# Kernel tuning notes

Hardware: AMD Instinct MI355X
Metric: run time of the kernel (lower is better)

Reference implementation:

```python
import jax, jax.numpy as jnp
import numpy as np

N = 100000      # nodes
E = 1600000     # edges (avg degree 16)
D_IN, D_HID, D_OUT = 128, 64, 32


def setup_inputs() -> dict:
    key = jax.random.key(0)
    ks = jax.random.split(key, 11)
    g = lambda k, shape, fan: jax.random.normal(k, shape, jnp.float32) * (1.0 / np.sqrt(fan))
    return {
        "x": jax.random.normal(ks[0], (N, D_IN), jnp.float32),
        "edges_index": jax.random.randint(ks[1], (2, E), 0, N, dtype=jnp.int64),
        # GATConv layer 1 (heads=1): linear weight, attention vectors a_src/a_dst, bias
        "W1": g(ks[2], (D_IN, D_HID), D_IN),
        "a_src1": g(ks[3], (D_HID,), D_HID),
        "a_dst1": g(ks[4], (D_HID,), D_HID),
        "b1": jnp.zeros((D_HID,), jnp.float32),
        # GATConv layer 2
        "W2": g(ks[5], (D_HID, D_OUT), D_HID),
        "a_src2": g(ks[6], (D_OUT,), D_OUT),
        "a_dst2": g(ks[7], (D_OUT,), D_OUT),
        "b2": jnp.zeros((D_OUT,), jnp.float32),
    }


def _gat_conv(x, src, dst, W, a_src, a_dst, b, n):
    """Single-head PyG GATConv: transform, edge attention, per-dst softmax, scatter-add."""
    h = x @ W                                        # [N, D]
    e = jax.nn.leaky_relu((h @ a_src)[src] + (h @ a_dst)[dst], 0.2)  # [E']
    # segment softmax over edges grouped by destination node
    m = jax.ops.segment_max(e, dst, num_segments=n)  # [N]
    w = jnp.exp(e - m[dst])                          # [E']
    s = jax.ops.segment_sum(w, dst, num_segments=n)  # [N]
    att = w / (s[dst] + 1e-16)                       # [E']
    out = jax.ops.segment_sum(att[:, None] * h[src], dst, num_segments=n)  # [N, D]
    return out + b


def reference(x, edges_index, W1, a_src1, a_dst1, b1, W2, a_src2, a_dst2, b2):
    n = x.shape[0]
    loops = jnp.arange(n, dtype=edges_index.dtype)   # GATConv add_self_loops=True
    src = jnp.concatenate([edges_index[0], loops])
    dst = jnp.concatenate([edges_index[1], loops])
    h = jax.nn.relu(_gat_conv(x, src, dst, W1, a_src1, a_dst1, b1, n))
    # F.dropout with training=False is identity (eval mode)
    out = _gat_conv(h, src, dst, W2, a_src2, a_dst2, b2, n)
    return jax.nn.log_softmax(out, axis=1)
```

## Files before the change

kernel.cpp:

```cpp
#include <hip/hip_runtime.h>
#include <math.h>

#define D_IN 128
#define D_HID 64
#define D_OUT 32
#define CAP 48
#define BSH 8
#define NB 391
#define CAPB 4608
#define CHUNK 8192
#define NPW 4

typedef __fp16 half2f __attribute__((ext_vector_type(2)));

__device__ __forceinline__ half2f u2h2(unsigned u) {
    union { unsigned u; half2f h; } c; c.u = u; return c.h;
}
__device__ __forceinline__ unsigned h22u(half2f h) {
    union { half2f h; unsigned u; } c; c.h = h; return c.u;
}
__device__ __forceinline__ unsigned short f2h(float f) {
    union { _Float16 h; unsigned short u; } c; c.h = (_Float16)f; return c.u;
}

#if defined(__has_builtin)
#  if __has_builtin(__builtin_amdgcn_fdot2)
#    define HAVE_FDOT2 1
#  else
#    define HAVE_FDOT2 0
#  endif
#else
#  define HAVE_FDOT2 0
#endif

__device__ __forceinline__ float fdot2f(half2f a, half2f b, float c) {
#if HAVE_FDOT2
    return __builtin_amdgcn_fdot2(a, b, c, false);
#else
    return fmaf((float)a.y, (float)b.y, fmaf((float)a.x, (float)b.x, c));
#endif
}

__device__ __forceinline__ void pair_acc(float wA, float wB, uint2 hA, uint2 hB,
                                         float& a0, float& a1, float& a2, float& a3)
{
    half2f wp = __builtin_amdgcn_cvt_pkrtz(wA, wB);
    a0 = fdot2f(wp, u2h2(__builtin_amdgcn_perm(hB.x, hA.x, 0x05040100u)), a0);
    a1 = fdot2f(wp, u2h2(__builtin_amdgcn_perm(hB.x, hA.x, 0x07060302u)), a1);
    a2 = fdot2f(wp, u2h2(__builtin_amdgcn_perm(hB.y, hA.y, 0x05040100u)), a2);
    a3 = fdot2f(wp, u2h2(__builtin_amdgcn_perm(hB.y, hA.y, 0x07060302u)), a3);
}


__global__ __launch_bounds__(256) void init_kernel(
    int* __restrict__ cnt, int* __restrict__ cursor, int n)
{
    int i = blockIdx.x * 256 + threadIdx.x;
    if (i < n) cnt[i] = 0;
    if (i < NB) cursor[i] = i * CAPB;
}

__global__ __launch_bounds__(256) void part_kernel(
    const int* __restrict__ esrc, const int* __restrict__ edst,
    unsigned long long* __restrict__ ebuf, int* __restrict__ cursor,
    int E, int Et)
{
    __shared__ int hist[NB];
    __shared__ int ofs[NB];
    const int t = threadIdx.x;
    const int base = blockIdx.x * CHUNK;
    const int end = min(base + CHUNK, Et);

    for (int b = t; b < NB; b += 256) hist[b] = 0;
    __syncthreads();
    for (int i = base + t; i < end; i += 256) {
        int d = (i < E) ? edst[i] : (i - E);
        atomicAdd(&hist[d >> BSH], 1);
    }
    __syncthreads();
    for (int b = t; b < NB; b += 256) {
        int c = hist[b];
        ofs[b] = c ? atomicAdd(&cursor[b], c) : 0;
    }
    __syncthreads();
    for (int i = base + t; i < end; i += 256) {
        int d = (i < E) ? edst[i] : (i - E);
        int s = (i < E) ? esrc[i] : (i - E);
        int p = atomicAdd(&ofs[d >> BSH], 1);
        ebuf[p] = ((unsigned long long)(unsigned)s << 32) | (unsigned)d;
    }
}

__global__ __launch_bounds__(256) void fill_bucket_kernel(
    const unsigned long long* __restrict__ ebuf, const int* __restrict__ cursor,
    int* __restrict__ cnt, int* __restrict__ csr_pad)
{
    int b = blockIdx.x;
    int beg = b * CAPB;
    int end = cursor[b];
    for (int i = beg + threadIdx.x; i < end; i += 256) {
        unsigned long long v = ebuf[i];
        int d = (int)(v & 0xffffffffu);
        int s = (int)(v >> 32);
        int slot = atomicAdd(&cnt[d], 1);
        if (slot < CAP) csr_pad[(size_t)d * CAP + slot] = s;
    }
}


template<int K, int NC, int RT, int PAD>
__global__ __launch_bounds__(256) void gemm_alpha_kernel(
    const float* __restrict__ A, const float* __restrict__ W,
    const float* __restrict__ a_src, const float* __restrict__ a_dst,
    unsigned short* __restrict__ C, float* __restrict__ as_,
    float* __restrict__ ad_, int M)
{
    constexpr int TM = 64;
    constexpr int CT = 4;
    constexpr int CG = NC / CT;
    constexpr int KS = K + PAD;
    __shared__ float xs[TM * KS];
    __shared__ float ws[K * NC];
    const int t = threadIdx.x;

    for (int i = t; i < K * NC / 4; i += 256)
        ((float4*)ws)[i] = ((const float4*)W)[i];

    const int base = blockIdx.x * TM;
    for (int i = t; i < TM * K / 4; i += 256) {
        int nloc = i / (K / 4);
        int k4   = i % (K / 4);
        int row  = base + nloc;
        float4 v = make_float4(0.f, 0.f, 0.f, 0.f);
        if (row < M)
            v = *(const float4*)(A + (size_t)row * K + k4 * 4);
        *(float4*)(xs + nloc * KS + k4 * 4) = v;
    }
    __syncthreads();

    const int tx = t % CG, ty = t / CG;
    const int r0 = ty * RT, c0 = tx * CT;
    float acc[RT][CT];
#pragma unroll
    for (int i = 0; i < RT; ++i)
#pragma unroll
        for (int j = 0; j < CT; ++j) acc[i][j] = 0.f;

    for (int k = 0; k < K; k += 4) {
        float4 a[RT];
#pragma unroll
        for (int i = 0; i < RT; ++i)
            a[i] = *(const float4*)(xs + (r0 + i) * KS + k);
#pragma unroll
        for (int kk = 0; kk < 4; ++kk) {
            float4 b = *(const float4*)(ws + (k + kk) * NC + c0);
#pragma unroll
            for (int i = 0; i < RT; ++i) {
                float av = kk == 0 ? a[i].x : kk == 1 ? a[i].y :
                           kk == 2 ? a[i].z : a[i].w;
                acc[i][0] = fmaf(av, b.x, acc[i][0]);
                acc[i][1] = fmaf(av, b.y, acc[i][1]);
                acc[i][2] = fmaf(av, b.z, acc[i][2]);
                acc[i][3] = fmaf(av, b.w, acc[i][3]);
            }
        }
    }

    const float4 asv = *(const float4*)(a_src + c0);
    const float4 adv = *(const float4*)(a_dst + c0);
#pragma unroll
    for (int i = 0; i < RT; ++i) {
        int row = base + r0 + i;
        float ps = acc[i][0] * asv.x + acc[i][1] * asv.y +
                   acc[i][2] * asv.z + acc[i][3] * asv.w;
        float pd = acc[i][0] * adv.x + acc[i][1] * adv.y +
                   acc[i][2] * adv.z + acc[i][3] * adv.w;
#pragma unroll
        for (int o = 1; o < CG; o <<= 1) {
            ps += __shfl_xor(ps, o);
            pd += __shfl_xor(pd, o);
        }
        if (row < M) {
            uint2 cv;
            cv.x = h22u(__builtin_amdgcn_cvt_pkrtz(acc[i][0], acc[i][1]));
            cv.y = h22u(__builtin_amdgcn_cvt_pkrtz(acc[i][2], acc[i][3]));
            *(uint2*)(C + (size_t)row * NC + c0) = cv;
            if (tx == 0) { as_[row] = ps; ad_[row] = pd; }
        }
    }
}

__global__ __launch_bounds__(256) void gat_aggr_fused_kernel(
    const int* __restrict__ cnt, const int* __restrict__ csr_pad,
    const float* __restrict__ as1, const float* __restrict__ ad1,
    const unsigned short* __restrict__ h1, const float* __restrict__ b1,
    const float* __restrict__ W2, const float* __restrict__ a2s,
    const float* __restrict__ a2d, unsigned short* __restrict__ h2,
    float* __restrict__ as2, float* __restrict__ ad2, int n)
{
    __shared__ float rbuf[4][64];
    const int t = threadIdx.x;
    const int wave = t >> 6;
    const int lane = t & 63;
    const int half = lane >> 5, j = lane & 31;

    float w2r[32];
#pragma unroll
    for (int k = 0; k < 32; ++k)
        w2r[k] = W2[(size_t)(half * 32 + k) * D_OUT + j];
    const float a2sj = a2s[j], a2dj = a2d[j];

    const int sub = lane >> 4;
    const int q4 = (lane & 15) * 4;
    const unsigned short* hq = h1 + q4;
    const float4 b1v = *(const float4*)(b1 + q4);

    const int d0 = (blockIdx.x * 4 + wave) * NPW;
    for (int it = 0; it < NPW; ++it) {
        const int d = d0 + it;
        if (d >= n) break;
        const int deg = min(cnt[d], CAP);
        const float add = ad1[d];

        int s = 0; float e = -1e30f;
        if (lane < deg) {
            s = csr_pad[(size_t)d * CAP + lane];
            float ev = as1[s] + add;
            e = (ev > 0.f) ? ev : 0.2f * ev;
        }
        float m = e;
#pragma unroll
        for (int o = 32; o > 0; o >>= 1) m = fmaxf(m, __shfl_xor(m, o));
        float w = __expf(e - m);
        float ssum = w;

        float a0 = 0.f, a1 = 0.f, a2v = 0.f, a3 = 0.f;
        {
            const int i0 = sub;
            float wA = __shfl(w, i0),      wB = __shfl(w, i0 + 4);
            float wC = __shfl(w, i0 + 8),  wD = __shfl(w, i0 + 12);
            int   sA = __shfl(s, i0),      sB = __shfl(s, i0 + 4);
            int   sC = __shfl(s, i0 + 8),  sD = __shfl(s, i0 + 12);
            uint2 hA = *(const uint2*)(hq + (size_t)sA * 64);
            uint2 hB = *(const uint2*)(hq + (size_t)sB * 64);
            uint2 hC = *(const uint2*)(hq + (size_t)sC * 64);
            uint2 hD = *(const uint2*)(hq + (size_t)sD * 64);
            if (deg > 16) {
                float wE = __shfl(w, i0 + 16), wF = __shfl(w, i0 + 20);
                float wG = __shfl(w, i0 + 24), wH = __shfl(w, i0 + 28);
                int   sE = __shfl(s, i0 + 16), sF = __shfl(s, i0 + 20);
                int   sG = __shfl(s, i0 + 24), sH = __shfl(s, i0 + 28);
                uint2 hE = *(const uint2*)(hq + (size_t)sE * 64);
                uint2 hF = *(const uint2*)(hq + (size_t)sF * 64);
                uint2 hG = *(const uint2*)(hq + (size_t)sG * 64);
                uint2 hH = *(const uint2*)(hq + (size_t)sH * 64);
                pair_acc(wA, wB, hA, hB, a0, a1, a2v, a3);
                pair_acc(wC, wD, hC, hD, a0, a1, a2v, a3);
                pair_acc(wE, wF, hE, hF, a0, a1, a2v, a3);
                pair_acc(wG, wH, hG, hH, a0, a1, a2v, a3);
            } else {
                pair_acc(wA, wB, hA, hB, a0, a1, a2v, a3);
                pair_acc(wC, wD, hC, hD, a0, a1, a2v, a3);
            }
        }
        if (deg > 32) {
            for (int tt = 32; tt < deg; tt += 16) {
                const int i0 = tt + sub;
                float wA = __shfl(w, i0),     wB = __shfl(w, i0 + 4);
                float wC = __shfl(w, i0 + 8), wD = __shfl(w, i0 + 12);
                int   sA = __shfl(s, i0),     sB = __shfl(s, i0 + 4);
                int   sC = __shfl(s, i0 + 8), sD = __shfl(s, i0 + 12);
                uint2 hA = *(const uint2*)(hq + (size_t)sA * 64);
                uint2 hB = *(const uint2*)(hq + (size_t)sB * 64);
                uint2 hC = *(const uint2*)(hq + (size_t)sC * 64);
                uint2 hD = *(const uint2*)(hq + (size_t)sD * 64);
                pair_acc(wA, wB, hA, hB, a0, a1, a2v, a3);
                pair_acc(wC, wD, hC, hD, a0, a1, a2v, a3);
            }
        }

#pragma unroll
        for (int o = 16; o <= 32; o <<= 1) {
            a0 += __shfl_xor(a0, o);  a1 += __shfl_xor(a1, o);
            a2v += __shfl_xor(a2v, o); a3 += __shfl_xor(a3, o);
        }
#pragma unroll
        for (int o = 32; o > 0; o >>= 1) ssum += __shfl_xor(ssum, o);

        const float inv = 1.0f / (ssum + 1e-16f);
        float4 rv;
        rv.x = fmaxf(fmaf(a0, inv, b1v.x), 0.f);
        rv.y = fmaxf(fmaf(a1, inv, b1v.y), 0.f);
        rv.z = fmaxf(fmaf(a2v, inv, b1v.z), 0.f);
        rv.w = fmaxf(fmaf(a3, inv, b1v.w), 0.f);
        if (sub == 0) *(float4*)(&rbuf[wave][q4]) = rv;

        const float* rb = &rbuf[wave][half * 32];
        float acc2 = 0.f;
#pragma unroll
        for (int k4 = 0; k4 < 8; ++k4) {
            float4 r4 = *(const float4*)(rb + k4 * 4);
            acc2 = fmaf(r4.x, w2r[k4 * 4 + 0], acc2);
            acc2 = fmaf(r4.y, w2r[k4 * 4 + 1], acc2);
            acc2 = fmaf(r4.z, w2r[k4 * 4 + 2], acc2);
            acc2 = fmaf(r4.w, w2r[k4 * 4 + 3], acc2);
        }
        acc2 += __shfl_xor(acc2, 32);

        float p1 = acc2 * a2sj, p2 = acc2 * a2dj;
#pragma unroll
        for (int o = 16; o > 0; o >>= 1) {
            p1 += __shfl_xor(p1, o);
            p2 += __shfl_xor(p2, o);
        }
        if (lane < 32) h2[(size_t)d * 32 + j] = f2h(acc2);
        if (lane == 0) { as2[d] = p1; ad2[d] = p2; }
    }
}

__global__ __launch_bounds__(256) void gat_aggr32_lsm_kernel(
    const int* __restrict__ cnt, const int* __restrict__ csr_pad,
    const float* __restrict__ as_, const float* __restrict__ ad_,
    const unsigned short* __restrict__ h, const float* __restrict__ bias,
    float* __restrict__ out, int n)
{
    int wave = threadIdx.x >> 6;
    int lane = threadIdx.x & 63;
    int d = blockIdx.x * 4 + wave;
    if (d >= n) return;
    int deg = min(cnt[d], CAP);
    float add = ad_[d];

    int s = 0; float e = -1e30f;
    if (lane < deg) {
        s = csr_pad[(size_t)d * CAP + lane];
        float ev = as_[s] + add;
        e = (ev > 0.f) ? ev : 0.2f * ev;
    }
    float m = e;
#pragma unroll
    for (int o = 32; o > 0; o >>= 1) m = fmaxf(m, __shfl_xor(m, o));
    float w = __expf(e - m);
    float ssum = w;

    const int sub = lane >> 3;
    const int q4 = (lane & 7) * 4;
    const unsigned short* hq = h + q4;
    float a0 = 0.f, a1 = 0.f, a2v = 0.f, a3 = 0.f;
    {
        const int i0 = sub;
        float wA = __shfl(w, i0),      wB = __shfl(w, i0 + 8);
        int   sA = __shfl(s, i0),      sB = __shfl(s, i0 + 8);
        uint2 hA = *(const uint2*)(hq + (size_t)sA * 32);
        uint2 hB = *(const uint2*)(hq + (size_t)sB * 32);
        if (deg > 16) {
            float wC = __shfl(w, i0 + 16), wD = __shfl(w, i0 + 24);
            int   sC = __shfl(s, i0 + 16), sD = __shfl(s, i0 + 24);
            uint2 hC = *(const uint2*)(hq + (size_t)sC * 32);
            uint2 hD = *(const uint2*)(hq + (size_t)sD * 32);
            pair_acc(wA, wB, hA, hB, a0, a1, a2v, a3);
            pair_acc(wC, wD, hC, hD, a0, a1, a2v, a3);
        } else {
            pair_acc(wA, wB, hA, hB, a0, a1, a2v, a3);
        }
    }
    if (deg > 32) {
        for (int tt = 32; tt < deg; tt += 16) {
            const int i0 = tt + sub;
            float wA = __shfl(w, i0), wB = __shfl(w, i0 + 8);
            int   sA = __shfl(s, i0), sB = __shfl(s, i0 + 8);
            uint2 hA = *(const uint2*)(hq + (size_t)sA * 32);
            uint2 hB = *(const uint2*)(hq + (size_t)sB * 32);
            pair_acc(wA, wB, hA, hB, a0, a1, a2v, a3);
        }
    }
#pragma unroll
    for (int o = 8; o <= 32; o <<= 1) {
        a0 += __shfl_xor(a0, o);  a1 += __shfl_xor(a1, o);
        a2v += __shfl_xor(a2v, o); a3 += __shfl_xor(a3, o);
    }
#pragma unroll
    for (int o = 32; o > 0; o >>= 1) ssum += __shfl_xor(ssum, o);

    float inv = 1.0f / (ssum + 1e-16f);
    const float4 bv = *(const float4*)(bias + q4);
    float r0 = fmaf(a0, inv, bv.x), r1 = fmaf(a1, inv, bv.y);
    float r2 = fmaf(a2v, inv, bv.z), r3 = fmaf(a3, inv, bv.w);

    float mx = fmaxf(fmaxf(r0, r1), fmaxf(r2, r3));
#pragma unroll
    for (int o = 1; o <= 4; o <<= 1) mx = fmaxf(mx, __shfl_xor(mx, o));
    float sm = __expf(r0 - mx) + __expf(r1 - mx) +
               __expf(r2 - mx) + __expf(r3 - mx);
#pragma unroll
    for (int o = 1; o <= 4; o <<= 1) sm += __shfl_xor(sm, o);
    float lg = mx + __logf(sm);
    if (sub == 0) {
        float4 ov = make_float4(r0 - lg, r1 - lg, r2 - lg, r3 - lg);
        *(float4*)(out + (size_t)d * 32 + q4) = ov;
    }
}

extern "C" void kernel_launch(void* const* d_in, const int* in_sizes, int n_in,
                              void* d_out, int out_size, void* d_ws, size_t ws_size,
                              hipStream_t stream) {
    const float* x    = (const float*)d_in[0];
    const int*   ei   = (const int*)  d_in[1];
    const float* W1   = (const float*)d_in[2];
    const float* av1s = (const float*)d_in[3];
    const float* av1d = (const float*)d_in[4];
    const float* b1   = (const float*)d_in[5];
    const float* W2   = (const float*)d_in[6];
    const float* av2s = (const float*)d_in[7];
    const float* av2d = (const float*)d_in[8];
    const float* b2   = (const float*)d_in[9];
    float* out = (float*)d_out;

    const int N  = in_sizes[0] / D_IN;
    const int E  = in_sizes[1] / 2;
    const int Et = E + N;
    const int* esrc = ei;
    const int* edst = ei + E;

    float* ws = (float*)d_ws;
    size_t off = 0;
    unsigned short* h1f = (unsigned short*)(ws + off); off += (size_t)N * 32;
    unsigned short* h2f_ = (unsigned short*)(ws + off); off += (size_t)N * 16;
    float* as1_ = ws + off;               off += N;
    float* ad1_ = ws + off;               off += N;
    float* as2_ = ws + off;               off += N;
    float* ad2_ = ws + off;               off += N;
    int* cnt    = (int*)(ws + off);       off += N;
    int* cursor = (int*)(ws + off);       off += NB + 1;
    int* csr_pad = (int*)(ws + off);      off += (size_t)N * CAP;
    if (off & 1) off++;
    unsigned long long* ebuf = (unsigned long long*)(ws + off);
    off += (size_t)NB * CAPB * 2;

    const int tiles  = (N + 63) / 64;
    const int nblk   = (N + 255) / 256;
    const int aggblk = (N + 3) / 4;
    const int fblk   = (N + 4 * NPW - 1) / (4 * NPW);
    const int pblk   = (Et + CHUNK - 1) / CHUNK;

    init_kernel<<<nblk, 256, 0, stream>>>(cnt, cursor, N);
    part_kernel<<<pblk, 256, 0, stream>>>(esrc, edst, ebuf, cursor, E, Et);
    fill_bucket_kernel<<<NB, 256, 0, stream>>>(ebuf, cursor, cnt, csr_pad);

    gemm_alpha_kernel<128, 64, 4, 0><<<tiles, 256, 0, stream>>>(
        x, W1, av1s, av1d, h1f, as1_, ad1_, N);

    gat_aggr_fused_kernel<<<fblk, 256, 0, stream>>>(
        cnt, csr_pad, as1_, ad1_, h1f, b1,
        W2, av2s, av2d, h2f_, as2_, ad2_, N);

    gat_aggr32_lsm_kernel<<<aggblk, 256, 0, stream>>>(
        cnt, csr_pad, as2_, ad2_, h2f_, b2, out, N);
}
```

Baseline: 311.6 us.

## Process two destination nodes per wave to overlap gather latency

```diff
diff --git a/kernel.cpp b/kernel.cpp
--- a/kernel.cpp
+++ b/kernel.cpp
@@ -9,7 +9,6 @@
 #define NB 391
 #define CAPB 4608
 #define CHUNK 8192
-#define NPW 4
 
 typedef __fp16 half2f __attribute__((ext_vector_type(2)));
 
@@ -198,7 +197,7 @@
     const float* __restrict__ a2d, unsigned short* __restrict__ h2,
     float* __restrict__ as2, float* __restrict__ ad2, int n)
 {
-    __shared__ float rbuf[4][64];
+    __shared__ float rbuf[4][2][64];
     const int t = threadIdx.x;
     const int wave = t >> 6;
     const int lane = t & 63;
@@ -215,106 +214,173 @@
     const unsigned short* hq = h1 + q4;
     const float4 b1v = *(const float4*)(b1 + q4);
 
-    const int d0 = (blockIdx.x * 4 + wave) * NPW;
-    for (int it = 0; it < NPW; ++it) {
-        const int d = d0 + it;
-        if (d >= n) break;
-        const int deg = min(cnt[d], CAP);
-        const float add = ad1[d];
-
-        int s = 0; float e = -1e30f;
-        if (lane < deg) {
-            s = csr_pad[(size_t)d * CAP + lane];
-            float ev = as1[s] + add;
-            e = (ev > 0.f) ? ev : 0.2f * ev;
-        }
-        float m = e;
-#pragma unroll
-        for (int o = 32; o > 0; o >>= 1) m = fmaxf(m, __shfl_xor(m, o));
-        float w = __expf(e - m);
-        float ssum = w;
-
-        float a0 = 0.f, a1 = 0.f, a2v = 0.f, a3 = 0.f;
-        {
-            const int i0 = sub;
-            float wA = __shfl(w, i0),      wB = __shfl(w, i0 + 4);
-            float wC = __shfl(w, i0 + 8),  wD = __shfl(w, i0 + 12);
-            int   sA = __shfl(s, i0),      sB = __shfl(s, i0 + 4);
-            int   sC = __shfl(s, i0 + 8),  sD = __shfl(s, i0 + 12);
-            uint2 hA = *(const uint2*)(hq + (size_t)sA * 64);
-            uint2 hB = *(const uint2*)(hq + (size_t)sB * 64);
-            uint2 hC = *(const uint2*)(hq + (size_t)sC * 64);
-            uint2 hD = *(const uint2*)(hq + (size_t)sD * 64);
-            if (deg > 16) {
-                float wE = __shfl(w, i0 + 16), wF = __shfl(w, i0 + 20);
-                float wG = __shfl(w, i0 + 24), wH = __shfl(w, i0 + 28);
-                int   sE = __shfl(s, i0 + 16), sF = __shfl(s, i0 + 20);
-                int   sG = __shfl(s, i0 + 24), sH = __shfl(s, i0 + 28);
-                uint2 hE = *(const uint2*)(hq + (size_t)sE * 64);
-                uint2 hF = *(const uint2*)(hq + (size_t)sF * 64);
-                uint2 hG = *(const uint2*)(hq + (size_t)sG * 64);
-                uint2 hH = *(const uint2*)(hq + (size_t)sH * 64);
-                pair_acc(wA, wB, hA, hB, a0, a1, a2v, a3);
-                pair_acc(wC, wD, hC, hD, a0, a1, a2v, a3);
-                pair_acc(wE, wF, hE, hF, a0, a1, a2v, a3);
-                pair_acc(wG, wH, hG, hH, a0, a1, a2v, a3);
-            } else {
-                pair_acc(wA, wB, hA, hB, a0, a1, a2v, a3);
-                pair_acc(wC, wD, hC, hD, a0, a1, a2v, a3);
-            }
-        }
-        if (deg > 32) {
-            for (int tt = 32; tt < deg; tt += 16) {
-                const int i0 = tt + sub;
-                float wA = __shfl(w, i0),     wB = __shfl(w, i0 + 4);
-                float wC = __shfl(w, i0 + 8), wD = __shfl(w, i0 + 12);
-                int   sA = __shfl(s, i0),     sB = __shfl(s, i0 + 4);
-                int   sC = __shfl(s, i0 + 8), sD = __shfl(s, i0 + 12);
-                uint2 hA = *(const uint2*)(hq + (size_t)sA * 64);
-                uint2 hB = *(const uint2*)(hq + (size_t)sB * 64);
-                uint2 hC = *(const uint2*)(hq + (size_t)sC * 64);
-                uint2 hD = *(const uint2*)(hq + (size_t)sD * 64);
-                pair_acc(wA, wB, hA, hB, a0, a1, a2v, a3);
-                pair_acc(wC, wD, hC, hD, a0, a1, a2v, a3);
-            }
-        }
-
-#pragma unroll
-        for (int o = 16; o <= 32; o <<= 1) {
-            a0 += __shfl_xor(a0, o);  a1 += __shfl_xor(a1, o);
-            a2v += __shfl_xor(a2v, o); a3 += __shfl_xor(a3, o);
-        }
-#pragma unroll
-        for (int o = 32; o > 0; o >>= 1) ssum += __shfl_xor(ssum, o);
-
-        const float inv = 1.0f / (ssum + 1e-16f);
-        float4 rv;
-        rv.x = fmaxf(fmaf(a0, inv, b1v.x), 0.f);
-        rv.y = fmaxf(fmaf(a1, inv, b1v.y), 0.f);
-        rv.z = fmaxf(fmaf(a2v, inv, b1v.z), 0.f);
-        rv.w = fmaxf(fmaf(a3, inv, b1v.w), 0.f);
-        if (sub == 0) *(float4*)(&rbuf[wave][q4]) = rv;
-
-        const float* rb = &rbuf[wave][half * 32];
-        float acc2 = 0.f;
-#pragma unroll
-        for (int k4 = 0; k4 < 8; ++k4) {
-            float4 r4 = *(const float4*)(rb + k4 * 4);
-            acc2 = fmaf(r4.x, w2r[k4 * 4 + 0], acc2);
-            acc2 = fmaf(r4.y, w2r[k4 * 4 + 1], acc2);
-            acc2 = fmaf(r4.z, w2r[k4 * 4 + 2], acc2);
-            acc2 = fmaf(r4.w, w2r[k4 * 4 + 3], acc2);
-        }
-        acc2 += __shfl_xor(acc2, 32);
-
-        float p1 = acc2 * a2sj, p2 = acc2 * a2dj;
-#pragma unroll
-        for (int o = 16; o > 0; o >>= 1) {
-            p1 += __shfl_xor(p1, o);
-            p2 += __shfl_xor(p2, o);
-        }
-        if (lane < 32) h2[(size_t)d * 32 + j] = f2h(acc2);
-        if (lane == 0) { as2[d] = p1; ad2[d] = p2; }
+    const int dA = (blockIdx.x * 4 + wave) * 2;
+    if (dA >= n) return;
+    const int dB = dA + 1;
+    const bool vB = dB < n;
+    const int dBe = vB ? dB : dA;
+
+    const int degA = min(cnt[dA], CAP);
+    const int degB = min(cnt[dBe], CAP);
+    const float addA = ad1[dA], addB = ad1[dBe];
+
+    int sA = 0, sB = 0; float eA = -1e30f, eB = -1e30f;
+    if (lane < degA) sA = csr_pad[(size_t)dA  * CAP + lane];
+    if (lane < degB) sB = csr_pad[(size_t)dBe * CAP + lane];
+    if (lane < degA) { float ev = as1[sA] + addA; eA = (ev > 0.f) ? ev : 0.2f * ev; }
+    if (lane < degB) { float ev = as1[sB] + addB; eB = (ev > 0.f) ? ev : 0.2f * ev; }
+
+    float mA = eA, mB = eB;
+#pragma unroll
+    for (int o = 32; o > 0; o >>= 1) {
+        mA = fmaxf(mA, __shfl_xor(mA, o));
+        mB = fmaxf(mB, __shfl_xor(mB, o));
+    }
+    float wA_ = __expf(eA - mA), wB_ = __expf(eB - mB);
+    float ssA = wA_, ssB = wB_;
+
+    float a0A = 0.f, a1A = 0.f, a2A = 0.f, a3A = 0.f;
+    float a0B = 0.f, a1B = 0.f, a2B = 0.f, a3B = 0.f;
+    {
+        const int i0 = sub;
+        float wa0 = __shfl(wA_, i0),      wa1 = __shfl(wA_, i0 + 4);
+        float wa2 = __shfl(wA_, i0 + 8),  wa3 = __shfl(wA_, i0 + 12);
+        float wa4 = __shfl(wA_, i0 + 16), wa5 = __shfl(wA_, i0 + 20);
+        float wa6 = __shfl(wA_, i0 + 24), wa7 = __shfl(wA_, i0 + 28);
+        int   sa0 = __shfl(sA, i0),       sa1 = __shfl(sA, i0 + 4);
+        int   sa2 = __shfl(sA, i0 + 8),   sa3 = __shfl(sA, i0 + 12);
+        int   sa4 = __shfl(sA, i0 + 16),  sa5 = __shfl(sA, i0 + 20);
+        int   sa6 = __shfl(sA, i0 + 24),  sa7 = __shfl(sA, i0 + 28);
+        float wb0 = __shfl(wB_, i0),      wb1 = __shfl(wB_, i0 + 4);
+        float wb2 = __shfl(wB_, i0 + 8),  wb3 = __shfl(wB_, i0 + 12);
+        float wb4 = __shfl(wB_, i0 + 16), wb5 = __shfl(wB_, i0 + 20);
+        float wb6 = __shfl(wB_, i0 + 24), wb7 = __shfl(wB_, i0 + 28);
+        int   sb0 = __shfl(sB, i0),       sb1 = __shfl(sB, i0 + 4);
+        int   sb2 = __shfl(sB, i0 + 8),   sb3 = __shfl(sB, i0 + 12);
+        int   sb4 = __shfl(sB, i0 + 16),  sb5 = __shfl(sB, i0 + 20);
+        int   sb6 = __shfl(sB, i0 + 24),  sb7 = __shfl(sB, i0 + 28);
+        uint2 ha0 = *(const uint2*)(hq + (size_t)sa0 * 64);
+        uint2 ha1 = *(const uint2*)(hq + (size_t)sa1 * 64);
+        uint2 ha2 = *(const uint2*)(hq + (size_t)sa2 * 64);
+        uint2 ha3 = *(const uint2*)(hq + (size_t)sa3 * 64);
+        uint2 ha4 = *(const uint2*)(hq + (size_t)sa4 * 64);
+        uint2 ha5 = *(const uint2*)(hq + (size_t)sa5 * 64);
+        uint2 ha6 = *(const uint2*)(hq + (size_t)sa6 * 64);
+        uint2 ha7 = *(const uint2*)(hq + (size_t)sa7 * 64);
+        uint2 hb0 = *(const uint2*)(hq + (size_t)sb0 * 64);
+        uint2 hb1 = *(const uint2*)(hq + (size_t)sb1 * 64);
+        uint2 hb2 = *(const uint2*)(hq + (size_t)sb2 * 64);
+        uint2 hb3 = *(const uint2*)(hq + (size_t)sb3 * 64);
+        uint2 hb4 = *(const uint2*)(hq + (size_t)sb4 * 64);
+        uint2 hb5 = *(const uint2*)(hq + (size_t)sb5 * 64);
+        uint2 hb6 = *(const uint2*)(hq + (size_t)sb6 * 64);
+        uint2 hb7 = *(const uint2*)(hq + (size_t)sb7 * 64);
+        pair_acc(wa0, wa1, ha0, ha1, a0A, a1A, a2A, a3A);
+        pair_acc(wa2, wa3, ha2, ha3, a0A, a1A, a2A, a3A);
+        pair_acc(wa4, wa5, ha4, ha5, a0A, a1A, a2A, a3A);
+        pair_acc(wa6, wa7, ha6, ha7, a0A, a1A, a2A, a3A);
+        pair_acc(wb0, wb1, hb0, hb1, a0B, a1B, a2B, a3B);
+        pair_acc(wb2, wb3, hb2, hb3, a0B, a1B, a2B, a3B);
+        pair_acc(wb4, wb5, hb4, hb5, a0B, a1B, a2B, a3B);
+        pair_acc(wb6, wb7, hb6, hb7, a0B, a1B, a2B, a3B);
+    }
+    if (degA > 32) {
+        for (int tt = 32; tt < degA; tt += 16) {
+            const int i0 = tt + sub;
+            float w0 = __shfl(wA_, i0),     w1 = __shfl(wA_, i0 + 4);
+            float w2 = __shfl(wA_, i0 + 8), w3 = __shfl(wA_, i0 + 12);
+            int   s0 = __shfl(sA, i0),      s1 = __shfl(sA, i0 + 4);
+            int   s2 = __shfl(sA, i0 + 8),  s3 = __shfl(sA, i0 + 12);
+            uint2 h0 = *(const uint2*)(hq + (size_t)s0 * 64);
+            uint2 h1_ = *(const uint2*)(hq + (size_t)s1 * 64);
+            uint2 h2_ = *(const uint2*)(hq + (size_t)s2 * 64);
+            uint2 h3_ = *(const uint2*)(hq + (size_t)s3 * 64);
+            pair_acc(w0, w1, h0, h1_, a0A, a1A, a2A, a3A);
+            pair_acc(w2, w3, h2_, h3_, a0A, a1A, a2A, a3A);
+        }
+    }
+    if (degB > 32) {
+        for (int tt = 32; tt < degB; tt += 16) {
+            const int i0 = tt + sub;
+            float w0 = __shfl(wB_, i0),     w1 = __shfl(wB_, i0 + 4);
+            float w2 = __shfl(wB_, i0 + 8), w3 = __shfl(wB_, i0 + 12);
+            int   s0 = __shfl(sB, i0),      s1 = __shfl(sB, i0 + 4);
+            int   s2 = __shfl(sB, i0 + 8),  s3 = __shfl(sB, i0 + 12);
+            uint2 h0 = *(const uint2*)(hq + (size_t)s0 * 64);
+            uint2 h1_ = *(const uint2*)(hq + (size_t)s1 * 64);
+            uint2 h2_ = *(const uint2*)(hq + (size_t)s2 * 64);
+            uint2 h3_ = *(const uint2*)(hq + (size_t)s3 * 64);
+            pair_acc(w0, w1, h0, h1_, a0B, a1B, a2B, a3B);
+            pair_acc(w2, w3, h2_, h3_, a0B, a1B, a2B, a3B);
+        }
+    }
+
+#pragma unroll
+    for (int o = 16; o <= 32; o <<= 1) {
+        a0A += __shfl_xor(a0A, o); a1A += __shfl_xor(a1A, o);
+        a2A += __shfl_xor(a2A, o); a3A += __shfl_xor(a3A, o);
+        a0B += __shfl_xor(a0B, o); a1B += __shfl_xor(a1B, o);
+        a2B += __shfl_xor(a2B, o); a3B += __shfl_xor(a3B, o);
+    }
+#pragma unroll
+    for (int o = 32; o > 0; o >>= 1) {
+        ssA += __shfl_xor(ssA, o);
+        ssB += __shfl_xor(ssB, o);
+    }
+
+    const float invA = 1.0f / (ssA + 1e-16f);
+    const float invB = 1.0f / (ssB + 1e-16f);
+    float4 rvA, rvB;
+    rvA.x = fmaxf(fmaf(a0A, invA, b1v.x), 0.f);
+    rvA.y = fmaxf(fmaf(a1A, invA, b1v.y), 0.f);
+    rvA.z = fmaxf(fmaf(a2A, invA, b1v.z), 0.f);
+    rvA.w = fmaxf(fmaf(a3A, invA, b1v.w), 0.f);
+    rvB.x = fmaxf(fmaf(a0B, invB, b1v.x), 0.f);
+    rvB.y = fmaxf(fmaf(a1B, invB, b1v.y), 0.f);
+    rvB.z = fmaxf(fmaf(a2B, invB, b1v.z), 0.f);
+    rvB.w = fmaxf(fmaf(a3B, invB, b1v.w), 0.f);
+    if (sub == 0) {
+        *(float4*)(&rbuf[wave][0][q4]) = rvA;
+        *(float4*)(&rbuf[wave][1][q4]) = rvB;
+    }
+
+    const float* rbA = &rbuf[wave][0][half * 32];
+    const float* rbB = &rbuf[wave][1][half * 32];
+    float acc2A = 0.f, acc2B = 0.f;
+#pragma unroll
+    for (int k4 = 0; k4 < 8; ++k4) {
+        float4 rA = *(const float4*)(rbA + k4 * 4);
+        float4 rB = *(const float4*)(rbB + k4 * 4);
+        acc2A = fmaf(rA.x, w2r[k4 * 4 + 0], acc2A);
+        acc2A = fmaf(rA.y, w2r[k4 * 4 + 1], acc2A);
+        acc2A = fmaf(rA.z, w2r[k4 * 4 + 2], acc2A);
+        acc2A = fmaf(rA.w, w2r[k4 * 4 + 3], acc2A);
+        acc2B = fmaf(rB.x, w2r[k4 * 4 + 0], acc2B);
+        acc2B = fmaf(rB.y, w2r[k4 * 4 + 1], acc2B);
+        acc2B = fmaf(rB.z, w2r[k4 * 4 + 2], acc2B);
+        acc2B = fmaf(rB.w, w2r[k4 * 4 + 3], acc2B);
+    }
+    acc2A += __shfl_xor(acc2A, 32);
+    acc2B += __shfl_xor(acc2B, 32);
+
+    float p1A = acc2A * a2sj, p2A = acc2A * a2dj;
+    float p1B = acc2B * a2sj, p2B = acc2B * a2dj;
+#pragma unroll
+    for (int o = 16; o > 0; o >>= 1) {
+        p1A += __shfl_xor(p1A, o); p2A += __shfl_xor(p2A, o);
+        p1B += __shfl_xor(p1B, o); p2B += __shfl_xor(p2B, o);
+    }
+    if (!half || vB) {
+        const int dd = half ? dBe : dA;
+        h2[(size_t)dd * 32 + j] = f2h(half ? acc2B : acc2A);
+    }
+    if (lane == 0) {
+        if (vB) {
+            *(float2*)(as2 + dA) = make_float2(p1A, p1B);
+            *(float2*)(ad2 + dA) = make_float2(p2A, p2B);
+        } else {
+            as2[dA] = p1A; ad2[dA] = p2A;
+        }
     }
 }
 
@@ -324,80 +390,126 @@
     const unsigned short* __restrict__ h, const float* __restrict__ bias,
     float* __restrict__ out, int n)
 {
-    int wave = threadIdx.x >> 6;
-    int lane = threadIdx.x & 63;
-    int d = blockIdx.x * 4 + wave;
-    if (d >= n) return;
-    int deg = min(cnt[d], CAP);
-    float add = ad_[d];
-
-    int s = 0; float e = -1e30f;
-    if (lane < deg) {
-        s = csr_pad[(size_t)d * CAP + lane];
-        float ev = as_[s] + add;
-        e = (ev > 0.f) ? ev : 0.2f * ev;
-    }
-    float m = e;
-#pragma unroll
-    for (int o = 32; o > 0; o >>= 1) m = fmaxf(m, __shfl_xor(m, o));
-    float w = __expf(e - m);
-    float ssum = w;
+    const int wave = threadIdx.x >> 6;
+    const int lane = threadIdx.x & 63;
+    const int dA = (blockIdx.x * 4 + wave) * 2;
+    if (dA >= n) return;
+    const int dB = dA + 1;
+    const bool vB = dB < n;
+    const int dBe = vB ? dB : dA;
+
+    const int degA = min(cnt[dA], CAP);
+    const int degB = min(cnt[dBe], CAP);
+    const float addA = ad_[dA], addB = ad_[dBe];
+
+    int sA = 0, sB = 0; float eA = -1e30f, eB = -1e30f;
+    if (lane < degA) sA = csr_pad[(size_t)dA  * CAP + lane];
+    if (lane < degB) sB = csr_pad[(size_t)dBe * CAP + lane];
+    if (lane < degA) { float ev = as_[sA] + addA; eA = (ev > 0.f) ? ev : 0.2f * ev; }
+    if (lane < degB) { float ev = as_[sB] + addB; eB = (ev > 0.f) ? ev : 0.2f * ev; }
+
+    float mA = eA, mB = eB;
+#pragma unroll
+    for (int o = 32; o > 0; o >>= 1) {
+        mA = fmaxf(mA, __shfl_xor(mA, o));
+        mB = fmaxf(mB, __shfl_xor(mB, o));
+    }
+    float wA_ = __expf(eA - mA), wB_ = __expf(eB - mB);
+    float ssA = wA_, ssB = wB_;
 
     const int sub = lane >> 3;
     const int q4 = (lane & 7) * 4;
     const unsigned short* hq = h + q4;
-    float a0 = 0.f, a1 = 0.f, a2v = 0.f, a3 = 0.f;
+    float a0A = 0.f, a1A = 0.f, a2A = 0.f, a3A = 0.f;
+    float a0B = 0.f, a1B = 0.f, a2B = 0.f, a3B = 0.f;
     {
         const int i0 = sub;
-        float wA = __shfl(w, i0),      wB = __shfl(w, i0 + 8);
-        int   sA = __shfl(s, i0),      sB = __shfl(s, i0 + 8);
-        uint2 hA = *(const uint2*)(hq + (size_t)sA * 32);
-        uint2 hB = *(const uint2*)(hq + (size_t)sB * 32);
-        if (deg > 16) {
-            float wC = __shfl(w, i0 + 16), wD = __shfl(w, i0 + 24);
-            int   sC = __shfl(s, i0 + 16), sD = __shfl(s, i0 + 24);
-            uint2 hC = *(const uint2*)(hq + (size_t)sC * 32);
-            uint2 hD = *(const uint2*)(hq + (size_t)sD * 32);
-            pair_acc(wA, wB, hA, hB, a0, a1, a2v, a3);
-            pair_acc(wC, wD, hC, hD, a0, a1, a2v, a3);
-        } else {
-            pair_acc(wA, wB, hA, hB, a0, a1, a2v, a3);
-        }
-    }
-    if (deg > 32) {
-        for (int tt = 32; tt < deg; tt += 16) {
+        float wa0 = __shfl(wA_, i0),      wa1 = __shfl(wA_, i0 + 8);
+        float wa2 = __shfl(wA_, i0 + 16), wa3 = __shfl(wA_, i0 + 24);
+        int   sa0 = __shfl(sA, i0),       sa1 = __shfl(sA, i0 + 8);
+        int   sa2 = __shfl(sA, i0 + 16),  sa3 = __shfl(sA, i0 + 24);
+        float wb0 = __shfl(wB_, i0),      wb1 = __shfl(wB_, i0 + 8);
+        float wb2 = __shfl(wB_, i0 + 16), wb3 = __shfl(wB_, i0 + 24);
+        int   sb0 = __shfl(sB, i0),       sb1 = __shfl(sB, i0 + 8);
+        int   sb2 = __shfl(sB, i0 + 16),  sb3 = __shfl(sB, i0 + 24);
+        uint2 ha0 = *(const uint2*)(hq + (size_t)sa0 * 32);
+        uint2 ha1 = *(const uint2*)(hq + (size_t)sa1 * 32);
+        uint2 ha2 = *(const uint2*)(hq + (size_t)sa2 * 32);
+        uint2 ha3 = *(const uint2*)(hq + (size_t)sa3 * 32);
+        uint2 hb0 = *(const uint2*)(hq + (size_t)sb0 * 32);
+        uint2 hb1 = *(const uint2*)(hq + (size_t)sb1 * 32);
+        uint2 hb2 = *(const uint2*)(hq + (size_t)sb2 * 32);
+        uint2 hb3 = *(const uint2*)(hq + (size_t)sb3 * 32);
+        pair_acc(wa0, wa1, ha0, ha1, a0A, a1A, a2A, a3A);
+        pair_acc(wa2, wa3, ha2, ha3, a0A, a1A, a2A, a3A);
+        pair_acc(wb0, wb1, hb0, hb1, a0B, a1B, a2B, a3B);
+        pair_acc(wb2, wb3, hb2, hb3, a0B, a1B, a2B, a3B);
+    }
+    if (degA > 32) {
+        for (int tt = 32; tt < degA; tt += 16) {
             const int i0 = tt + sub;
-            float wA = __shfl(w, i0), wB = __shfl(w, i0 + 8);
-            int   sA = __shfl(s, i0), sB = __shfl(s, i0 + 8);
-            uint2 hA = *(const uint2*)(hq + (size_t)sA * 32);
-            uint2 hB = *(const uint2*)(hq + (size_t)sB * 32);
-            pair_acc(wA, wB, hA, hB, a0, a1, a2v, a3);
+            float w0 = __shfl(wA_, i0); float w1 = __shfl(wA_, i0 + 8);
+            int   s0 = __shfl(sA, i0);  int   s1 = __shfl(sA, i0 + 8);
+            uint2 h0 = *(const uint2*)(hq + (size_t)s0 * 32);
+            uint2 h1_ = *(const uint2*)(hq + (size_t)s1 * 32);
+            pair_acc(w0, w1, h0, h1_, a0A, a1A, a2A, a3A);
+        }
+    }
+    if (degB > 32) {
+        for (int tt = 32; tt < degB; tt += 16) {
+            const int i0 = tt + sub;
+            float w0 = __shfl(wB_, i0); float w1 = __shfl(wB_, i0 + 8);
+            int   s0 = __shfl(sB, i0);  int   s1 = __shfl(sB, i0 + 8);
+            uint2 h0 = *(const uint2*)(hq + (size_t)s0 * 32);
+            uint2 h1_ = *(const uint2*)(hq + (size_t)s1 * 32);
+            pair_acc(w0, w1, h0, h1_, a0B, a1B, a2B, a3B);
         }
     }
 #pragma unroll
     for (int o = 8; o <= 32; o <<= 1) {
-        a0 += __shfl_xor(a0, o);  a1 += __shfl_xor(a1, o);
-        a2v += __shfl_xor(a2v, o); a3 += __shfl_xor(a3, o);
-    }
-#pragma unroll
-    for (int o = 32; o > 0; o >>= 1) ssum += __shfl_xor(ssum, o);
-
-    float inv = 1.0f / (ssum + 1e-16f);
+        a0A += __shfl_xor(a0A, o); a1A += __shfl_xor(a1A, o);
+        a2A += __shfl_xor(a2A, o); a3A += __shfl_xor(a3A, o);
+        a0B += __shfl_xor(a0B, o); a1B += __shfl_xor(a1B, o);
+        a2B += __shfl_xor(a2B, o); a3B += __shfl_xor(a3B, o);
+    }
+#pragma unroll
+    for (int o = 32; o > 0; o >>= 1) {
+        ssA += __shfl_xor(ssA, o);
+        ssB += __shfl_xor(ssB, o);
+    }
+
+    const float invA = 1.0f / (ssA + 1e-16f);
+    const float invB = 1.0f / (ssB + 1e-16f);
     const float4 bv = *(const float4*)(bias + q4);
-    float r0 = fmaf(a0, inv, bv.x), r1 = fmaf(a1, inv, bv.y);
-    float r2 = fmaf(a2v, inv, bv.z), r3 = fmaf(a3, inv, bv.w);
-
-    float mx = fmaxf(fmaxf(r0, r1), fmaxf(r2, r3));
-#pragma unroll
-    for (int o = 1; o <= 4; o <<= 1) mx = fmaxf(mx, __shfl_xor(mx, o));
-    float sm = __expf(r0 - mx) + __expf(r1 - mx) +
-               __expf(r2 - mx) + __expf(r3 - mx);
-#pragma unroll
-    for (int o = 1; o <= 4; o <<= 1) sm += __shfl_xor(sm, o);
-    float lg = mx + __logf(sm);
+    float r0A = fmaf(a0A, invA, bv.x), r1A = fmaf(a1A, invA, bv.y);
+    float r2A = fmaf(a2A, invA, bv.z), r3A = fmaf(a3A, invA, bv.w);
+    float r0B = fmaf(a0B, invB, bv.x), r1B = fmaf(a1B, invB, bv.y);
+    float r2B = fmaf(a2B, invB, bv.z), r3B = fmaf(a3B, invB, bv.w);
+
+    float mxA = fmaxf(fmaxf(r0A, r1A), fmaxf(r2A, r3A));
+    float mxB = fmaxf(fmaxf(r0B, r1B), fmaxf(r2B, r3B));
+#pragma unroll
+    for (int o = 1; o <= 4; o <<= 1) {
+        mxA = fmaxf(mxA, __shfl_xor(mxA, o));
+        mxB = fmaxf(mxB, __shfl_xor(mxB, o));
+    }
+    float smA = __expf(r0A - mxA) + __expf(r1A - mxA) +
+                __expf(r2A - mxA) + __expf(r3A - mxA);
+    float smB = __expf(r0B - mxB) + __expf(r1B - mxB) +
+                __expf(r2B - mxB) + __expf(r3B - mxB);
+#pragma unroll
+    for (int o = 1; o <= 4; o <<= 1) {
+        smA += __shfl_xor(smA, o);
+        smB += __shfl_xor(smB, o);
+    }
+    float lgA = mxA + __logf(smA);
+    float lgB = mxB + __logf(smB);
     if (sub == 0) {
-        float4 ov = make_float4(r0 - lg, r1 - lg, r2 - lg, r3 - lg);
-        *(float4*)(out + (size_t)d * 32 + q4) = ov;
+        float4 ov = make_float4(r0A - lgA, r1A - lgA, r2A - lgA, r3A - lgA);
+        *(float4*)(out + (size_t)dA * 32 + q4) = ov;
+    } else if (sub == 1 && vB) {
+        float4 ov = make_float4(r0B - lgB, r1B - lgB, r2B - lgB, r3B - lgB);
+        *(float4*)(out + (size_t)dB * 32 + q4) = ov;
     }
 }
 
@@ -439,8 +551,7 @@
 
     const int tiles  = (N + 63) / 64;
     const int nblk   = (N + 255) / 256;
-    const int aggblk = (N + 3) / 4;
-    const int fblk   = (N + 4 * NPW - 1) / (4 * NPW);
+    const int pairblk = (N + 7) / 8;
     const int pblk   = (Et + CHUNK - 1) / CHUNK;
 
     init_kernel<<<nblk, 256, 0, stream>>>(cnt, cursor, N);
@@ -450,10 +561,10 @@
     gemm_alpha_kernel<128, 64, 4, 0><<<tiles, 256, 0, stream>>>(
         x, W1, av1s, av1d, h1f, as1_, ad1_, N);
 
-    gat_aggr_fused_kernel<<<fblk, 256, 0, stream>>>(
+    gat_aggr_fused_kernel<<<pairblk, 256, 0, stream>>>(
         cnt, csr_pad, as1_, ad1_, h1f, b1,
         W2, av2s, av2d, h2f_, as2_, ad2_, N);
 
-    gat_aggr32_lsm_kernel<<<aggblk, 256, 0, stream>>>(
+    gat_aggr32_lsm_kernel<<<pairblk, 256, 0, stream>>>(
         cnt, csr_pad, as2_, ad2_, h2f_, b2, out, N);
 }
```

After: 320.6 us. +2.9%, slower.

## Software-prefetch next node's CSR indices and alpha in aggregation kernels

Applied to the files above, without the earlier changes.

```diff
diff --git a/kernel.cpp b/kernel.cpp
--- a/kernel.cpp
+++ b/kernel.cpp
@@ -216,23 +216,41 @@
     const float4 b1v = *(const float4*)(b1 + q4);
 
     const int d0 = (blockIdx.x * 4 + wave) * NPW;
+    if (d0 >= n) return;
+
+    int   deg_p = min(cnt[d0], CAP);
+    float add_p = ad1[d0];
+    int   s_p = 0; float araw_p = 0.f;
+    if (lane < deg_p) s_p = csr_pad[(size_t)d0 * CAP + lane];
+    if (lane < deg_p) araw_p = as1[s_p];
+
     for (int it = 0; it < NPW; ++it) {
         const int d = d0 + it;
         if (d >= n) break;
-        const int deg = min(cnt[d], CAP);
-        const float add = ad1[d];
-
-        int s = 0; float e = -1e30f;
-        if (lane < deg) {
-            s = csr_pad[(size_t)d * CAP + lane];
-            float ev = as1[s] + add;
-            e = (ev > 0.f) ? ev : 0.2f * ev;
-        }
+        const int   deg  = deg_p;
+        const float add  = add_p;
+        const int   s    = s_p;
+        const float araw = araw_p;
+
+        const int dn = d + 1;
+        const bool pf = (it + 1 < NPW) && (dn < n);
+        int deg_n = 0; float add_n = 0.f; int s_n = 0;
+        if (pf) {
+            deg_n = min(cnt[dn], CAP);
+            add_n = ad1[dn];
+            if (lane < deg_n) s_n = csr_pad[(size_t)dn * CAP + lane];
+        }
+
+        float e = -1e30f;
+        if (lane < deg) { float ev = araw + add; e = (ev > 0.f) ? ev : 0.2f * ev; }
         float m = e;
 #pragma unroll
         for (int o = 32; o > 0; o >>= 1) m = fmaxf(m, __shfl_xor(m, o));
         float w = __expf(e - m);
         float ssum = w;
+
+        float araw_n = 0.f;
+        if (pf && lane < deg_n) araw_n = as1[s_n];
 
         float a0 = 0.f, a1 = 0.f, a2v = 0.f, a3 = 0.f;
         {
@@ -315,6 +333,8 @@
         }
         if (lane < 32) h2[(size_t)d * 32 + j] = f2h(acc2);
         if (lane == 0) { as2[d] = p1; ad2[d] = p2; }
+
+        deg_p = deg_n; add_p = add_n; s_p = s_n; araw_p = araw_n;
     }
 }
 
@@ -324,80 +344,104 @@
     const unsigned short* __restrict__ h, const float* __restrict__ bias,
     float* __restrict__ out, int n)
 {
-    int wave = threadIdx.x >> 6;
-    int lane = threadIdx.x & 63;
-    int d = blockIdx.x * 4 + wave;
-    if (d >= n) return;
-    int deg = min(cnt[d], CAP);
-    float add = ad_[d];
-
-    int s = 0; float e = -1e30f;
-    if (lane < deg) {
-        s = csr_pad[(size_t)d * CAP + lane];
-        float ev = as_[s] + add;
-        e = (ev > 0.f) ? ev : 0.2f * ev;
-    }
-    float m = e;
-#pragma unroll
-    for (int o = 32; o > 0; o >>= 1) m = fmaxf(m, __shfl_xor(m, o));
-    float w = __expf(e - m);
-    float ssum = w;
+    const int wave = threadIdx.x >> 6;
+    const int lane = threadIdx.x & 63;
+    const int d0 = (blockIdx.x * 4 + wave) * NPW;
+    if (d0 >= n) return;
 
     const int sub = lane >> 3;
     const int q4 = (lane & 7) * 4;
     const unsigned short* hq = h + q4;
-    float a0 = 0.f, a1 = 0.f, a2v = 0.f, a3 = 0.f;
-    {
-        const int i0 = sub;
-        float wA = __shfl(w, i0),      wB = __shfl(w, i0 + 8);
-        int   sA = __shfl(s, i0),      sB = __shfl(s, i0 + 8);
-        uint2 hA = *(const uint2*)(hq + (size_t)sA * 32);
-        uint2 hB = *(const uint2*)(hq + (size_t)sB * 32);
-        if (deg > 16) {
-            float wC = __shfl(w, i0 + 16), wD = __shfl(w, i0 + 24);
-            int   sC = __shfl(s, i0 + 16), sD = __shfl(s, i0 + 24);
-            uint2 hC = *(const uint2*)(hq + (size_t)sC * 32);
-            uint2 hD = *(const uint2*)(hq + (size_t)sD * 32);
-            pair_acc(wA, wB, hA, hB, a0, a1, a2v, a3);
-            pair_acc(wC, wD, hC, hD, a0, a1, a2v, a3);
-        } else {
-            pair_acc(wA, wB, hA, hB, a0, a1, a2v, a3);
-        }
-    }
-    if (deg > 32) {
-        for (int tt = 32; tt < deg; tt += 16) {
-            const int i0 = tt + sub;
-            float wA = __shfl(w, i0), wB = __shfl(w, i0 + 8);
-            int   sA = __shfl(s, i0), sB = __shfl(s, i0 + 8);
+    const float4 bv = *(const float4*)(bias + q4);
+
+    int   deg_p = min(cnt[d0], CAP);
+    float add_p = ad_[d0];
+    int   s_p = 0; float araw_p = 0.f;
+    if (lane < deg_p) s_p = csr_pad[(size_t)d0 * CAP + lane];
+    if (lane < deg_p) araw_p = as_[s_p];
+
+    for (int it = 0; it < NPW; ++it) {
+        const int d = d0 + it;
+        if (d >= n) break;
+        const int   deg  = deg_p;
+        const float add  = add_p;
+        const int   s    = s_p;
+        const float araw = araw_p;
+
+        const int dn = d + 1;
+        const bool pf = (it + 1 < NPW) && (dn < n);
+        int deg_n = 0; float add_n = 0.f; int s_n = 0;
+        if (pf) {
+            deg_n = min(cnt[dn], CAP);
+            add_n = ad_[dn];
+            if (lane < deg_n) s_n = csr_pad[(size_t)dn * CAP + lane];
+        }
+
+        float e = -1e30f;
+        if (lane < deg) { float ev = araw + add; e = (ev > 0.f) ? ev : 0.2f * ev; }
+        float m = e;
+#pragma unroll
+        for (int o = 32; o > 0; o >>= 1) m = fmaxf(m, __shfl_xor(m, o));
+        float w = __expf(e - m);
+        float ssum = w;
+
+        float araw_n = 0.f;
+        if (pf && lane < deg_n) araw_n = as_[s_n];
+
+        float a0 = 0.f, a1 = 0.f, a2v = 0.f, a3 = 0.f;
+        {
+            const int i0 = sub;
+            float wA = __shfl(w, i0),      wB = __shfl(w, i0 + 8);
+            int   sA = __shfl(s, i0),      sB = __shfl(s, i0 + 8);
             uint2 hA = *(const uint2*)(hq + (size_t)sA * 32);
             uint2 hB = *(const uint2*)(hq + (size_t)sB * 32);
-            pair_acc(wA, wB, hA, hB, a0, a1, a2v, a3);
-        }
-    }
-#pragma unroll
-    for (int o = 8; o <= 32; o <<= 1) {
-        a0 += __shfl_xor(a0, o);  a1 += __shfl_xor(a1, o);
-        a2v += __shfl_xor(a2v, o); a3 += __shfl_xor(a3, o);
-    }
-#pragma unroll
-    for (int o = 32; o > 0; o >>= 1) ssum += __shfl_xor(ssum, o);
-
-    float inv = 1.0f / (ssum + 1e-16f);
-    const float4 bv = *(const float4*)(bias + q4);
-    float r0 = fmaf(a0, inv, bv.x), r1 = fmaf(a1, inv, bv.y);
-    float r2 = fmaf(a2v, inv, bv.z), r3 = fmaf(a3, inv, bv.w);
-
-    float mx = fmaxf(fmaxf(r0, r1), fmaxf(r2, r3));
-#pragma unroll
-    for (int o = 1; o <= 4; o <<= 1) mx = fmaxf(mx, __shfl_xor(mx, o));
-    float sm = __expf(r0 - mx) + __expf(r1 - mx) +
-               __expf(r2 - mx) + __expf(r3 - mx);
-#pragma unroll
-    for (int o = 1; o <= 4; o <<= 1) sm += __shfl_xor(sm, o);
-    float lg = mx + __logf(sm);
-    if (sub == 0) {
-        float4 ov = make_float4(r0 - lg, r1 - lg, r2 - lg, r3 - lg);
-        *(float4*)(out + (size_t)d * 32 + q4) = ov;
+            if (deg > 16) {
+                float wC = __shfl(w, i0 + 16), wD = __shfl(w, i0 + 24);
+                int   sC = __shfl(s, i0 + 16), sD = __shfl(s, i0 + 24);
+                uint2 hC = *(const uint2*)(hq + (size_t)sC * 32);
+                uint2 hD = *(const uint2*)(hq + (size_t)sD * 32);
+                pair_acc(wA, wB, hA, hB, a0, a1, a2v, a3);
+                pair_acc(wC, wD, hC, hD, a0, a1, a2v, a3);
+            } else {
+                pair_acc(wA, wB, hA, hB, a0, a1, a2v, a3);
+            }
+        }
+        if (deg > 32) {
+            for (int tt = 32; tt < deg; tt += 16) {
+                const int i0 = tt + sub;
+                float wA = __shfl(w, i0); float wB = __shfl(w, i0 + 8);
+                int   sA = __shfl(s, i0); int   sB = __shfl(s, i0 + 8);
+                uint2 hA = *(const uint2*)(hq + (size_t)sA * 32);
+                uint2 hB = *(const uint2*)(hq + (size_t)sB * 32);
+                pair_acc(wA, wB, hA, hB, a0, a1, a2v, a3);
+            }
+        }
+#pragma unroll
+        for (int o = 8; o <= 32; o <<= 1) {
+            a0 += __shfl_xor(a0, o);  a1 += __shfl_xor(a1, o);
+            a2v += __shfl_xor(a2v, o); a3 += __shfl_xor(a3, o);
+        }
+#pragma unroll
+        for (int o = 32; o > 0; o >>= 1) ssum += __shfl_xor(ssum, o);
+
+        float inv = 1.0f / (ssum + 1e-16f);
+        float r0 = fmaf(a0, inv, bv.x), r1 = fmaf(a1, inv, bv.y);
+        float r2 = fmaf(a2v, inv, bv.z), r3 = fmaf(a3, inv, bv.w);
+
+        float mx = fmaxf(fmaxf(r0, r1), fmaxf(r2, r3));
+#pragma unroll
+        for (int o = 1; o <= 4; o <<= 1) mx = fmaxf(mx, __shfl_xor(mx, o));
+        float sm = __expf(r0 - mx) + __expf(r1 - mx) +
+                   __expf(r2 - mx) + __expf(r3 - mx);
+#pragma unroll
+        for (int o = 1; o <= 4; o <<= 1) sm += __shfl_xor(sm, o);
+        float lg = mx + __logf(sm);
+        if (sub == 0) {
+            float4 ov = make_float4(r0 - lg, r1 - lg, r2 - lg, r3 - lg);
+            *(float4*)(out + (size_t)d * 32 + q4) = ov;
+        }
+
+        deg_p = deg_n; add_p = add_n; s_p = s_n; araw_p = araw_n;
     }
 }
 
@@ -439,8 +483,7 @@
 
     const int tiles  = (N + 63) / 64;
     const int nblk   = (N + 255) / 256;
-    const int aggblk = (N + 3) / 4;
-    const int fblk   = (N + 4 * NPW - 1) / (4 * NPW);
+    const int aggblk = (N + 4 * NPW - 1) / (4 * NPW);
     const int pblk   = (Et + CHUNK - 1) / CHUNK;
 
     init_kernel<<<nblk, 256, 0, stream>>>(cnt, cursor, N);
@@ -450,7 +493,7 @@
     gemm_alpha_kernel<128, 64, 4, 0><<<tiles, 256, 0, stream>>>(
         x, W1, av1s, av1d, h1f, as1_, ad1_, N);
 
-    gat_aggr_fused_kernel<<<fblk, 256, 0, stream>>>(
+    gat_aggr_fused_kernel<<<aggblk, 256, 0, stream>>>(
         cnt, csr_pad, as1_, ad1_, h1f, b1,
         W2, av2s, av2d, h2f_, as2_, ad2_, N);
 
```

Result: slower. 321.5 us (+3.2%).
